# Performance work log

Hardware: AMD Instinct MI355X
Metric: run time of the kernel (lower is better)

Reference implementation:

```python
import jax, jax.numpy as jnp
import numpy as np
from jax import lax

B, VLEN, H, DIM, C = 32, 2048, 1024, 1024, 32  # batch, value len, hidden_dim, dim, conv_out_channel


def setup_inputs() -> dict:
    key = jax.random.key(0)
    ks = jax.random.split(key, 13)
    s = 0.02
    return {
        "query": jax.random.normal(ks[0], (B, 1, H), dtype=jnp.float32),
        "value": jax.random.normal(ks[1], (B, VLEN, H), dtype=jnp.float32),
        "prev_attn": jax.random.uniform(ks[2], (B, VLEN), dtype=jnp.float32),
        "conv_w": jax.random.normal(ks[3], (C, 1, 3), dtype=jnp.float32) * s,   # Conv1d weight (out,in,k)
        "conv_b": jax.random.normal(ks[4], (C,), dtype=jnp.float32) * s,
        "w_loc": jax.random.normal(ks[5], (DIM, C), dtype=jnp.float32) * s,     # loc_projection (no bias)
        "w_q": jax.random.normal(ks[6], (DIM, H), dtype=jnp.float32) * s,       # query_projection (no bias)
        "w_v": jax.random.normal(ks[7], (DIM, H), dtype=jnp.float32) * s,       # value_projection (no bias)
        "bias": jax.random.uniform(ks[8], (DIM,), dtype=jnp.float32, minval=-0.1, maxval=0.1),
        "w_score": jax.random.normal(ks[9], (1, DIM), dtype=jnp.float32) * s,   # score_projection weight
        "b_score": jax.random.normal(ks[10], (1,), dtype=jnp.float32) * s,
        "w_out": jax.random.normal(ks[11], (H, 2 * H), dtype=jnp.float32) * s,  # out_projection weight
        "b_out": jax.random.normal(ks[12], (H,), dtype=jnp.float32) * s,
    }


def reference(query, value, prev_attn, conv_w, conv_b, w_loc, w_q, w_v, bias,
              w_score, b_score, w_out, b_out):
    # Location features: Conv1d(1 -> C, k=3, pad=1) over prev_attn, then transpose to (B, V, C)
    conv = lax.conv_general_dilated(
        prev_attn[:, None, :], conv_w, window_strides=(1,), padding=[(1, 1)],
        dimension_numbers=("NCH", "OIH", "NCH"),
    ) + conv_b[None, :, None]                       # (B, C, V)
    conv_feat = jnp.transpose(conv, (0, 2, 1))      # (B, V, C)

    qp = jnp.einsum("bqh,dh->bqd", query, w_q)      # (B, 1, DIM)
    vp = jnp.einsum("bvh,dh->bvd", value, w_v)      # (B, V, DIM)
    lp = jnp.einsum("bvc,dc->bvd", conv_feat, w_loc)

    e = jnp.tanh(qp + vp + lp + bias)               # (B, V, DIM), qp broadcasts over V
    score = jnp.einsum("bvd,d->bv", e, w_score[0]) + b_score[0]  # (B, V)

    # smoothing=True: sigmoid then normalize
    s = jax.nn.sigmoid(score)
    attn = s / jnp.sum(s, axis=-1, keepdims=True)   # (B, V)

    context = jnp.einsum("bv,bvh->bh", attn, value)               # (B, H)
    combined = jnp.concatenate([context[:, None, :], query], axis=2)  # (B, 1, 2H)
    output = jnp.einsum("bqk,hk->bqh", combined, w_out) + b_out       # (B, 1, H)
    return output, attn
```

## Files before the change

### kernel.cpp

```cpp
#include <hip/hip_runtime.h>
#include <hip/hip_bf16.h>
#include <math.h>

#define B_SZ 32
#define VLEN_SZ 2048
#define H_SZ 1024
#define DIM_SZ 1024
#define C_SZ 32

typedef float f32x4 __attribute__((ext_vector_type(4)));
typedef short s16x8 __attribute__((ext_vector_type(8)));
typedef short s16x4 __attribute__((ext_vector_type(4)));

__device__ __forceinline__ short f2bf(float f) {
  unsigned u = __float_as_uint(f);
  u = (u + 0x7fffu + ((u >> 16) & 1u)) >> 16;
  return (short)u;
}

__device__ __forceinline__ float bf2f(short s) {
  return __uint_as_float(((unsigned)(unsigned short)s) << 16);
}

__device__ __forceinline__ float fast_tanh(float x) {
  float z = __expf(2.0f * x);
  return 1.0f - 2.0f / (z + 1.0f);
}

__device__ __forceinline__ void ldg_lds16(const short* g, short* l) {
  __builtin_amdgcn_global_load_lds(
      (const __attribute__((address_space(1))) unsigned int*)g,
      (__attribute__((address_space(3))) unsigned int*)l, 16, 0, 0);
}

__global__ void k_qpb(const float* __restrict__ query, const float* __restrict__ w_q,
                      const float* __restrict__ bias, float* __restrict__ qpb) {
  int wid = blockIdx.x * 4 + (threadIdx.x >> 6);
  int lane = threadIdx.x & 63;
  int d = wid >> 5;
  int b = wid & 31;
  const f32x4* q4 = (const f32x4*)(query + (size_t)b * H_SZ);
  const f32x4* w4 = (const f32x4*)(w_q + (size_t)d * H_SZ);
  float acc = 0.f;
#pragma unroll
  for (int it = 0; it < 4; ++it) {
    int k = it * 64 + lane;
    f32x4 a = q4[k], w = w4[k];
    acc += a[0] * w[0] + a[1] * w[1] + a[2] * w[2] + a[3] * w[3];
  }
#pragma unroll
  for (int off = 32; off; off >>= 1) acc += __shfl_xor(acc, off, 64);
  if (lane == 0) qpb[(size_t)b * DIM_SZ + d] = acc + bias[d];
}

__global__ void k_f2bf(const float* __restrict__ src, short* __restrict__ dst, int n4) {
  int i = blockIdx.x * blockDim.x + threadIdx.x;
  if (i >= n4) return;
  f32x4 v = ((const f32x4*)src)[i];
  s16x4 o;
  o[0] = f2bf(v[0]); o[1] = f2bf(v[1]); o[2] = f2bf(v[2]); o[3] = f2bf(v[3]);
  ((s16x4*)dst)[i] = o;
}

__global__ void k_cast8(const float* __restrict__ src, short* __restrict__ dst) {
  size_t i = (size_t)blockIdx.x * 256 + threadIdx.x;
  f32x4 x0 = ((const f32x4*)src)[2 * i];
  f32x4 x1 = ((const f32x4*)src)[2 * i + 1];
  s16x8 o;
  o[0] = f2bf(x0[0]); o[1] = f2bf(x0[1]); o[2] = f2bf(x0[2]); o[3] = f2bf(x0[3]);
  o[4] = f2bf(x1[0]); o[5] = f2bf(x1[1]); o[6] = f2bf(x1[2]); o[7] = f2bf(x1[3]);
  ((s16x8*)dst)[i] = o;
}

__global__ void k_cf(const float* __restrict__ prev, const float* __restrict__ conv_w,
                     const float* __restrict__ conv_b, short* __restrict__ cfb) {
  int t = blockIdx.x * 256 + threadIdx.x;
  int v = t & (VLEN_SZ - 1);
  float p0 = prev[t];
  float pm = (v > 0) ? prev[t - 1] : 0.f;
  float pp = (v < VLEN_SZ - 1) ? prev[t + 1] : 0.f;
#pragma unroll
  for (int c = 0; c < C_SZ; ++c) {
    float f = conv_b[c] + pm * conv_w[c * 3 + 0] + p0 * conv_w[c * 3 + 1] + pp * conv_w[c * 3 + 2];
    cfb[(size_t)t * C_SZ + c] = f2bf(f);
  }
}

__global__ __launch_bounds__(256, 3) void k_score(
    const short* __restrict__ vb, const short* __restrict__ wvb,
    const short* __restrict__ wlocb, const short* __restrict__ cfb,
    const float* __restrict__ qpb, const float* __restrict__ w_score,
    float* __restrict__ score) {
  __shared__ short As[128 * 32];
  __shared__ short Bs[128 * 32];
  __shared__ float sred[4][64];

  int t = threadIdx.x;
  int w = t >> 6, l = t & 63;
  int q = l >> 4, l16 = l & 15;
  int nt = blockIdx.x;
  int mt = blockIdx.y;
  int row0 = mt * 128;
  int d0 = nt * 128;
  int b = row0 >> 11;
  int wm = w >> 1, wn = w & 1;

  int lr = l >> 2;
  int kc = ((l & 3) ^ ((l >> 3) & 3)) * 8;

  const short* gA0 = vb + (size_t)(row0 + 32 * w + lr) * H_SZ + kc;
  const short* gA1 = vb + (size_t)(row0 + 32 * w + 16 + lr) * H_SZ + kc;
  const short* gB0 = wvb + (size_t)(d0 + 32 * w + lr) * H_SZ + kc;
  const short* gB1 = wvb + (size_t)(d0 + 32 * w + 16 + lr) * H_SZ + kc;
  short* lA0 = As + (32 * w) * 32;
  short* lA1 = As + (32 * w + 16) * 32;
  short* lB0 = Bs + (32 * w) * 32;
  short* lB1 = Bs + (32 * w + 16) * 32;

  int posA = (q ^ ((l16 >> 1) & 3)) * 8;

  f32x4 acc[4][4];
#pragma unroll
  for (int i = 0; i < 4; ++i)
#pragma unroll
    for (int j = 0; j < 4; ++j) acc[i][j] = (f32x4){0.f, 0.f, 0.f, 0.f};

  for (int kt = 0; kt <= 32; ++kt) {
    if (kt < 32) {
      int k0 = kt * 32;
      ldg_lds16(gA0 + k0, lA0);
      ldg_lds16(gA1 + k0, lA1);
      ldg_lds16(gB0 + k0, lB0);
      ldg_lds16(gB1 + k0, lB1);
    } else {
      ldg_lds16(cfb + (size_t)(row0 + 32 * w + lr) * C_SZ + kc, lA0);
      ldg_lds16(cfb + (size_t)(row0 + 32 * w + 16 + lr) * C_SZ + kc, lA1);
      ldg_lds16(wlocb + (size_t)(d0 + 32 * w + lr) * C_SZ + kc, lB0);
      ldg_lds16(wlocb + (size_t)(d0 + 32 * w + 16 + lr) * C_SZ + kc, lB1);
    }
    __syncthreads();

    s16x8 a[4], bb[4];
#pragma unroll
    for (int i = 0; i < 4; ++i)
      a[i] = *(const s16x8*)(As + (wm * 64 + i * 16 + l16) * 32 + posA);
#pragma unroll
    for (int j = 0; j < 4; ++j)
      bb[j] = *(const s16x8*)(Bs + (wn * 64 + j * 16 + l16) * 32 + posA);
#pragma unroll
    for (int i = 0; i < 4; ++i)
#pragma unroll
      for (int j = 0; j < 4; ++j)
        acc[i][j] = __builtin_amdgcn_mfma_f32_16x16x32_bf16(a[i], bb[j], acc[i][j], 0, 0, 0);
    __syncthreads();
  }

  float qv[4], wv[4];
#pragma unroll
  for (int j = 0; j < 4; ++j) {
    int d = d0 + wn * 64 + j * 16 + l16;
    qv[j] = qpb[(size_t)b * DIM_SZ + d];
    wv[j] = w_score[d];
  }

#pragma unroll
  for (int i = 0; i < 4; ++i) {
#pragma unroll
    for (int r = 0; r < 4; ++r) {
      float part = 0.f;
#pragma unroll
      for (int j = 0; j < 4; ++j)
        part += fast_tanh(acc[i][j][r] + qv[j]) * wv[j];
      part += __shfl_xor(part, 1);
      part += __shfl_xor(part, 2);
      part += __shfl_xor(part, 4);
      part += __shfl_xor(part, 8);
      if (l16 == 0) sred[w][i * 16 + q * 4 + r] = part;
    }
  }
  __syncthreads();
  if (t < 128) {
    int half = t >> 6;
    float v = sred[half * 2][t & 63] + sred[half * 2 + 1][t & 63];
    atomicAdd(&score[row0 + t], v);
  }
}

__global__ void k_attn(const float* __restrict__ score, const float* __restrict__ b_score,
                       float* __restrict__ attn_out) {
  __shared__ float red[4];
  int b = blockIdx.x, t = threadIdx.x;
  float bs = b_score[0];
  float s[8];
  float sum = 0.f;
#pragma unroll
  for (int k = 0; k < 8; ++k) {
    float sc = score[(size_t)b * VLEN_SZ + k * 256 + t] + bs;
    s[k] = 1.0f / (1.0f + __expf(-sc));
    sum += s[k];
  }
#pragma unroll
  for (int off = 32; off; off >>= 1) sum += __shfl_xor(sum, off, 64);
  if ((t & 63) == 0) red[t >> 6] = sum;
  __syncthreads();
  float inv = 1.0f / (red[0] + red[1] + red[2] + red[3]);
#pragma unroll
  for (int k = 0; k < 8; ++k)
    attn_out[(size_t)b * VLEN_SZ + k * 256 + t] = s[k] * inv;
}

__global__ void k_ctx(const float* __restrict__ attn, const short* __restrict__ vb,
                      float* __restrict__ context) {
  __shared__ float al[512];
  int b = blockIdx.x, ht = blockIdx.y, vc = blockIdx.z, t = threadIdx.x;
  int v0 = vc * 512;
  al[t] = attn[(size_t)b * VLEN_SZ + v0 + t];
  al[t + 256] = attn[(size_t)b * VLEN_SZ + v0 + 256 + t];
  __syncthreads();
  int h = ht * 256 + t;
  const short* vp = vb + ((size_t)b * VLEN_SZ + v0) * H_SZ + h;
  float acc = 0.f;
#pragma unroll 8
  for (int v = 0; v < 512; ++v) acc += al[v] * bf2f(vp[(size_t)v * H_SZ]);
  atomicAdd(&context[(size_t)b * H_SZ + h], acc);
}

__global__ void k_out(const float* __restrict__ context, const float* __restrict__ query,
                      const float* __restrict__ w_out, const float* __restrict__ b_out,
                      float* __restrict__ out) {
  int wid = blockIdx.x * 4 + (threadIdx.x >> 6);
  int lane = threadIdx.x & 63;
  int h = wid >> 5;
  int b = wid & 31;
  const f32x4* w4 = (const f32x4*)(w_out + (size_t)h * 2048);
  const f32x4* c4 = (const f32x4*)(context + (size_t)b * H_SZ);
  const f32x4* q4 = (const f32x4*)(query + (size_t)b * H_SZ);
  float acc = 0.f;
#pragma unroll
  for (int it = 0; it < 8; ++it) {
    int k4 = it * 64 + lane;
    f32x4 w = w4[k4];
    f32x4 c = (k4 < 256) ? c4[k4] : q4[k4 - 256];
    acc += w[0] * c[0] + w[1] * c[1] + w[2] * c[2] + w[3] * c[3];
  }
#pragma unroll
  for (int off = 32; off; off >>= 1) acc += __shfl_xor(acc, off, 64);
  if (lane == 0) out[(size_t)b * H_SZ + h] = acc + b_out[h];
}

extern "C" void kernel_launch(void* const* d_in, const int* in_sizes, int n_in,
                              void* d_out, int out_size, void* d_ws, size_t ws_size,
                              hipStream_t stream) {
  const float* query   = (const float*)d_in[0];
  const float* value   = (const float*)d_in[1];
  const float* prev    = (const float*)d_in[2];
  const float* conv_w  = (const float*)d_in[3];
  const float* conv_b  = (const float*)d_in[4];
  const float* w_loc   = (const float*)d_in[5];
  const float* w_q     = (const float*)d_in[6];
  const float* w_v     = (const float*)d_in[7];
  const float* bias    = (const float*)d_in[8];
  const float* w_score = (const float*)d_in[9];
  const float* b_score = (const float*)d_in[10];
  const float* w_out   = (const float*)d_in[11];
  const float* b_out   = (const float*)d_in[12];

  float* out  = (float*)d_out;
  float* attn = out + B_SZ * H_SZ;

  char* ws = (char*)d_ws;
  float* score   = (float*)(ws);
  float* qpb     = (float*)(ws + (256 << 10));
  float* context = (float*)(ws + (384 << 10));
  short* wvb     = (short*)(ws + (512 << 10));
  short* wlocb   = (short*)(ws + (2560 << 10));
  short* cfb     = (short*)(ws + (3 << 20));
  short* vb      = (short*)(ws + (8 << 20));

  hipMemsetAsync(score, 0, B_SZ * VLEN_SZ * sizeof(float), stream);
  hipMemsetAsync(context, 0, B_SZ * H_SZ * sizeof(float), stream);

  k_cast8<<<(B_SZ * VLEN_SZ * H_SZ) / (256 * 8), 256, 0, stream>>>(value, vb);
  k_f2bf<<<1024, 256, 0, stream>>>(w_v, wvb, (DIM_SZ * H_SZ) / 4);
  k_f2bf<<<32, 256, 0, stream>>>(w_loc, wlocb, (DIM_SZ * C_SZ) / 4);
  k_cf<<<(B_SZ * VLEN_SZ) / 256, 256, 0, stream>>>(prev, conv_w, conv_b, cfb);
  k_qpb<<<(B_SZ * DIM_SZ) / 4, 256, 0, stream>>>(query, w_q, bias, qpb);
  k_score<<<dim3(8, 512), 256, 0, stream>>>(vb, wvb, wlocb, cfb, qpb, w_score, score);
  k_attn<<<B_SZ, 256, 0, stream>>>(score, b_score, attn);
  k_ctx<<<dim3(B_SZ, 4, 4), 256, 0, stream>>>(attn, vb, context);
  k_out<<<(B_SZ * H_SZ) / 4, 256, 0, stream>>>(context, query, w_out, b_out, out);
}
```

Measured before the change: 653.7 us.

## Fuse prep kernels, remap score grid for L2 reuse, fuse attn into ctx

Merges the casts, conv-feature, query-projection and zeroing work into one launch, replacing the memsets and several small kernels. The score GEMM grid becomes a 1D launch remapped so consecutive blocks cover all eight N tiles of the same row block, aiming for better L2 reuse of the value tiles. The sigmoid/normalisation step is folded into the context kernel. That kernel now reads 8 bf16 values per thread with vector loads and uses fewer blocks, each recomputing the per-batch sum. The cost is fewer context blocks (128), which may leave many CUs idle during that phase.

```diff
diff --git a/kernel.cpp b/kernel.cpp
--- a/kernel.cpp
+++ b/kernel.cpp
@@ -33,56 +33,71 @@
       (__attribute__((address_space(3))) unsigned int*)l, 16, 0, 0);
 }
 
-__global__ void k_qpb(const float* __restrict__ query, const float* __restrict__ w_q,
-                      const float* __restrict__ bias, float* __restrict__ qpb) {
-  int wid = blockIdx.x * 4 + (threadIdx.x >> 6);
-  int lane = threadIdx.x & 63;
-  int d = wid >> 5;
-  int b = wid & 31;
-  const f32x4* q4 = (const f32x4*)(query + (size_t)b * H_SZ);
-  const f32x4* w4 = (const f32x4*)(w_q + (size_t)d * H_SZ);
-  float acc = 0.f;
-#pragma unroll
-  for (int it = 0; it < 4; ++it) {
-    int k = it * 64 + lane;
-    f32x4 a = q4[k], w = w4[k];
-    acc += a[0] * w[0] + a[1] * w[1] + a[2] * w[2] + a[3] * w[3];
-  }
-#pragma unroll
-  for (int off = 32; off; off >>= 1) acc += __shfl_xor(acc, off, 64);
-  if (lane == 0) qpb[(size_t)b * DIM_SZ + d] = acc + bias[d];
-}
-
-__global__ void k_f2bf(const float* __restrict__ src, short* __restrict__ dst, int n4) {
-  int i = blockIdx.x * blockDim.x + threadIdx.x;
-  if (i >= n4) return;
-  f32x4 v = ((const f32x4*)src)[i];
-  s16x4 o;
-  o[0] = f2bf(v[0]); o[1] = f2bf(v[1]); o[2] = f2bf(v[2]); o[3] = f2bf(v[3]);
-  ((s16x4*)dst)[i] = o;
-}
-
-__global__ void k_cast8(const float* __restrict__ src, short* __restrict__ dst) {
-  size_t i = (size_t)blockIdx.x * 256 + threadIdx.x;
-  f32x4 x0 = ((const f32x4*)src)[2 * i];
-  f32x4 x1 = ((const f32x4*)src)[2 * i + 1];
-  s16x8 o;
-  o[0] = f2bf(x0[0]); o[1] = f2bf(x0[1]); o[2] = f2bf(x0[2]); o[3] = f2bf(x0[3]);
-  o[4] = f2bf(x1[0]); o[5] = f2bf(x1[1]); o[6] = f2bf(x1[2]); o[7] = f2bf(x1[3]);
-  ((s16x8*)dst)[i] = o;
-}
-
-__global__ void k_cf(const float* __restrict__ prev, const float* __restrict__ conv_w,
-                     const float* __restrict__ conv_b, short* __restrict__ cfb) {
-  int t = blockIdx.x * 256 + threadIdx.x;
-  int v = t & (VLEN_SZ - 1);
-  float p0 = prev[t];
-  float pm = (v > 0) ? prev[t - 1] : 0.f;
-  float pp = (v < VLEN_SZ - 1) ? prev[t + 1] : 0.f;
-#pragma unroll
-  for (int c = 0; c < C_SZ; ++c) {
-    float f = conv_b[c] + pm * conv_w[c * 3 + 0] + p0 * conv_w[c * 3 + 1] + pp * conv_w[c * 3 + 2];
-    cfb[(size_t)t * C_SZ + c] = f2bf(f);
+__global__ __launch_bounds__(256) void k_prep(
+    const float* __restrict__ query, const float* __restrict__ w_q,
+    const float* __restrict__ bias, const float* __restrict__ prev,
+    const float* __restrict__ conv_w, const float* __restrict__ conv_b,
+    const float* __restrict__ w_loc, const float* __restrict__ w_v,
+    const float* __restrict__ value,
+    float* __restrict__ qpb, short* __restrict__ cfb, short* __restrict__ wlocb,
+    short* __restrict__ wvb, short* __restrict__ vb,
+    float* __restrict__ score, float* __restrict__ context) {
+  int bid = blockIdx.x;
+  int t = threadIdx.x;
+  if (bid < 8192) {
+    int wid = bid * 4 + (t >> 6);
+    int lane = t & 63;
+    int d = wid >> 5;
+    int b = wid & 31;
+    const f32x4* q4 = (const f32x4*)(query + (size_t)b * H_SZ);
+    const f32x4* w4 = (const f32x4*)(w_q + (size_t)d * H_SZ);
+    float acc = 0.f;
+#pragma unroll
+    for (int it = 0; it < 4; ++it) {
+      int k = it * 64 + lane;
+      f32x4 a = q4[k], w = w4[k];
+      acc += a[0] * w[0] + a[1] * w[1] + a[2] * w[2] + a[3] * w[3];
+    }
+#pragma unroll
+    for (int off = 32; off; off >>= 1) acc += __shfl_xor(acc, off, 64);
+    if (lane == 0) qpb[(size_t)b * DIM_SZ + d] = acc + bias[d];
+  } else if (bid < 8448) {
+    int r = (bid - 8192) * 256 + t;
+    int v = r & (VLEN_SZ - 1);
+    float p0 = prev[r];
+    float pm = (v > 0) ? prev[r - 1] : 0.f;
+    float pp = (v < VLEN_SZ - 1) ? prev[r + 1] : 0.f;
+#pragma unroll
+    for (int c = 0; c < C_SZ; ++c) {
+      float f = conv_b[c] + pm * conv_w[c * 3 + 0] + p0 * conv_w[c * 3 + 1] + pp * conv_w[c * 3 + 2];
+      cfb[(size_t)r * C_SZ + c] = f2bf(f);
+    }
+  } else if (bid < 8480) {
+    int i = (bid - 8448) * 256 + t;
+    f32x4 v = ((const f32x4*)w_loc)[i];
+    s16x4 o;
+    o[0] = f2bf(v[0]); o[1] = f2bf(v[1]); o[2] = f2bf(v[2]); o[3] = f2bf(v[3]);
+    ((s16x4*)wlocb)[i] = o;
+  } else if (bid < 9504) {
+    int i = (bid - 8480) * 256 + t;
+    f32x4 v = ((const f32x4*)w_v)[i];
+    s16x4 o;
+    o[0] = f2bf(v[0]); o[1] = f2bf(v[1]); o[2] = f2bf(v[2]); o[3] = f2bf(v[3]);
+    ((s16x4*)wvb)[i] = o;
+  } else if (bid < 9568) {
+    int i = (bid - 9504) * 256 + t;
+    ((f32x4*)score)[i] = (f32x4){0.f, 0.f, 0.f, 0.f};
+  } else if (bid < 9600) {
+    int i = (bid - 9568) * 256 + t;
+    ((f32x4*)context)[i] = (f32x4){0.f, 0.f, 0.f, 0.f};
+  } else {
+    size_t i = (size_t)(bid - 9600) * 256 + t;
+    f32x4 x0 = ((const f32x4*)value)[2 * i];
+    f32x4 x1 = ((const f32x4*)value)[2 * i + 1];
+    s16x8 o;
+    o[0] = f2bf(x0[0]); o[1] = f2bf(x0[1]); o[2] = f2bf(x0[2]); o[3] = f2bf(x0[3]);
+    o[4] = f2bf(x1[0]); o[5] = f2bf(x1[1]); o[6] = f2bf(x1[2]); o[7] = f2bf(x1[3]);
+    ((s16x8*)vb)[i] = o;
   }
 }
 
@@ -98,8 +113,11 @@
   int t = threadIdx.x;
   int w = t >> 6, l = t & 63;
   int q = l >> 4, l16 = l & 15;
-  int nt = blockIdx.x;
-  int mt = blockIdx.y;
+  int bid = blockIdx.x;
+  int x = bid & 7;
+  int j = bid >> 3;
+  int nt = j & 7;
+  int mt = x * 64 + (j >> 3);
   int row0 = mt * 128;
   int d0 = nt * 128;
   int b = row0 >> 11;
@@ -123,7 +141,7 @@
 #pragma unroll
   for (int i = 0; i < 4; ++i)
 #pragma unroll
-    for (int j = 0; j < 4; ++j) acc[i][j] = (f32x4){0.f, 0.f, 0.f, 0.f};
+    for (int jj = 0; jj < 4; ++jj) acc[i][jj] = (f32x4){0.f, 0.f, 0.f, 0.f};
 
   for (int kt = 0; kt <= 32; ++kt) {
     if (kt < 32) {
@@ -145,22 +163,22 @@
     for (int i = 0; i < 4; ++i)
       a[i] = *(const s16x8*)(As + (wm * 64 + i * 16 + l16) * 32 + posA);
 #pragma unroll
-    for (int j = 0; j < 4; ++j)
-      bb[j] = *(const s16x8*)(Bs + (wn * 64 + j * 16 + l16) * 32 + posA);
+    for (int jj = 0; jj < 4; ++jj)
+      bb[jj] = *(const s16x8*)(Bs + (wn * 64 + jj * 16 + l16) * 32 + posA);
 #pragma unroll
     for (int i = 0; i < 4; ++i)
 #pragma unroll
-      for (int j = 0; j < 4; ++j)
-        acc[i][j] = __builtin_amdgcn_mfma_f32_16x16x32_bf16(a[i], bb[j], acc[i][j], 0, 0, 0);
+      for (int jj = 0; jj < 4; ++jj)
+        acc[i][jj] = __builtin_amdgcn_mfma_f32_16x16x32_bf16(a[i], bb[jj], acc[i][jj], 0, 0, 0);
     __syncthreads();
   }
 
   float qv[4], wv[4];
 #pragma unroll
-  for (int j = 0; j < 4; ++j) {
-    int d = d0 + wn * 64 + j * 16 + l16;
-    qv[j] = qpb[(size_t)b * DIM_SZ + d];
-    wv[j] = w_score[d];
+  for (int jj = 0; jj < 4; ++jj) {
+    int d = d0 + wn * 64 + jj * 16 + l16;
+    qv[jj] = qpb[(size_t)b * DIM_SZ + d];
+    wv[jj] = w_score[d];
   }
 
 #pragma unroll
@@ -169,8 +187,8 @@
     for (int r = 0; r < 4; ++r) {
       float part = 0.f;
 #pragma unroll
-      for (int j = 0; j < 4; ++j)
-        part += fast_tanh(acc[i][j][r] + qv[j]) * wv[j];
+      for (int jj = 0; jj < 4; ++jj)
+        part += fast_tanh(acc[i][jj][r] + qv[jj]) * wv[jj];
       part += __shfl_xor(part, 1);
       part += __shfl_xor(part, 2);
       part += __shfl_xor(part, 4);
@@ -186,43 +204,51 @@
   }
 }
 
-__global__ void k_attn(const float* __restrict__ score, const float* __restrict__ b_score,
-                       float* __restrict__ attn_out) {
+__global__ __launch_bounds__(256) void k_ctx(
+    const float* __restrict__ score, const float* __restrict__ b_score,
+    const short* __restrict__ vb, float* __restrict__ attn_out,
+    float* __restrict__ context) {
+  __shared__ float als[VLEN_SZ];
   __shared__ float red[4];
-  int b = blockIdx.x, t = threadIdx.x;
+  int b = blockIdx.x, vc = blockIdx.y, t = threadIdx.x;
   float bs = b_score[0];
-  float s[8];
-  float sum = 0.f;
+  float sv[8];
+  float lsum = 0.f;
+  int v0 = t * 8;
 #pragma unroll
   for (int k = 0; k < 8; ++k) {
-    float sc = score[(size_t)b * VLEN_SZ + k * 256 + t] + bs;
-    s[k] = 1.0f / (1.0f + __expf(-sc));
-    sum += s[k];
-  }
-#pragma unroll
-  for (int off = 32; off; off >>= 1) sum += __shfl_xor(sum, off, 64);
-  if ((t & 63) == 0) red[t >> 6] = sum;
+    float ps = score[(size_t)b * VLEN_SZ + v0 + k] + bs;
+    float s = 1.0f / (1.0f + __expf(-ps));
+    sv[k] = s;
+    lsum += s;
+    als[v0 + k] = s;
+  }
+#pragma unroll
+  for (int off = 32; off; off >>= 1) lsum += __shfl_xor(lsum, off, 64);
+  if ((t & 63) == 0) red[t >> 6] = lsum;
   __syncthreads();
   float inv = 1.0f / (red[0] + red[1] + red[2] + red[3]);
+  if (vc == 0) {
+#pragma unroll
+    for (int k = 0; k < 8; ++k)
+      attn_out[(size_t)b * VLEN_SZ + v0 + k] = sv[k] * inv;
+  }
+
+  int p = t >> 7, tt = t & 127, h0 = tt * 8;
+  int vbase = vc * 512 + p * 256;
+  const short* vp = vb + ((size_t)b * VLEN_SZ + vbase) * H_SZ + h0;
+  const float* av = als + vbase;
+  float acc[8] = {0.f, 0.f, 0.f, 0.f, 0.f, 0.f, 0.f, 0.f};
+#pragma unroll 4
+  for (int v = 0; v < 256; ++v) {
+    s16x8 xv = *(const s16x8*)(vp + (size_t)v * H_SZ);
+    float a = av[v];
+#pragma unroll
+    for (int k = 0; k < 8; ++k) acc[k] += a * bf2f(xv[k]);
+  }
 #pragma unroll
   for (int k = 0; k < 8; ++k)
-    attn_out[(size_t)b * VLEN_SZ + k * 256 + t] = s[k] * inv;
-}
-
-__global__ void k_ctx(const float* __restrict__ attn, const short* __restrict__ vb,
-                      float* __restrict__ context) {
-  __shared__ float al[512];
-  int b = blockIdx.x, ht = blockIdx.y, vc = blockIdx.z, t = threadIdx.x;
-  int v0 = vc * 512;
-  al[t] = attn[(size_t)b * VLEN_SZ + v0 + t];
-  al[t + 256] = attn[(size_t)b * VLEN_SZ + v0 + 256 + t];
-  __syncthreads();
-  int h = ht * 256 + t;
-  const short* vp = vb + ((size_t)b * VLEN_SZ + v0) * H_SZ + h;
-  float acc = 0.f;
-#pragma unroll 8
-  for (int v = 0; v < 512; ++v) acc += al[v] * bf2f(vp[(size_t)v * H_SZ]);
-  atomicAdd(&context[(size_t)b * H_SZ + h], acc);
+    atomicAdd(&context[(size_t)b * H_SZ + h0 + k], acc[k] * inv);
 }
 
 __global__ void k_out(const float* __restrict__ context, const float* __restrict__ query,
@@ -277,16 +303,10 @@
   short* cfb     = (short*)(ws + (3 << 20));
   short* vb      = (short*)(ws + (8 << 20));
 
-  hipMemsetAsync(score, 0, B_SZ * VLEN_SZ * sizeof(float), stream);
-  hipMemsetAsync(context, 0, B_SZ * H_SZ * sizeof(float), stream);
-
-  k_cast8<<<(B_SZ * VLEN_SZ * H_SZ) / (256 * 8), 256, 0, stream>>>(value, vb);
-  k_f2bf<<<1024, 256, 0, stream>>>(w_v, wvb, (DIM_SZ * H_SZ) / 4);
-  k_f2bf<<<32, 256, 0, stream>>>(w_loc, wlocb, (DIM_SZ * C_SZ) / 4);
-  k_cf<<<(B_SZ * VLEN_SZ) / 256, 256, 0, stream>>>(prev, conv_w, conv_b, cfb);
-  k_qpb<<<(B_SZ * DIM_SZ) / 4, 256, 0, stream>>>(query, w_q, bias, qpb);
-  k_score<<<dim3(8, 512), 256, 0, stream>>>(vb, wvb, wlocb, cfb, qpb, w_score, score);
-  k_attn<<<B_SZ, 256, 0, stream>>>(score, b_score, attn);
-  k_ctx<<<dim3(B_SZ, 4, 4), 256, 0, stream>>>(attn, vb, context);
+  k_prep<<<42368, 256, 0, stream>>>(query, w_q, bias, prev, conv_w, conv_b,
+                                    w_loc, w_v, value,
+                                    qpb, cfb, wlocb, wvb, vb, score, context);
+  k_score<<<4096, 256, 0, stream>>>(vb, wvb, wlocb, cfb, qpb, w_score, score);
+  k_ctx<<<dim3(B_SZ, 4), 256, 0, stream>>>(score, b_score, vb, attn, context);
   k_out<<<(B_SZ * H_SZ) / 4, 256, 0, stream>>>(context, query, w_out, b_out, out);
 }
```

Result: faster. 637.7 us (-2.4%).
